# Performance work log

Measured on AMD Instinct MI355X. Metric: run time of the kernel, lower is better.

## Reference

```python
import jax, jax.numpy as jnp
import numpy as np

N_NODES = 100000
N_FEAT = 500
N_HID = 16
N_CLS = 7
N_EDGES = 3200000


def setup_inputs() -> dict:
    key = jax.random.key(0)
    k1, k2, k3, k4 = jax.random.split(key, 4)
    x = jax.random.normal(k1, (N_NODES, N_FEAT), dtype=jnp.float32)
    edge_index = jax.random.randint(k2, (2, N_EDGES), 0, N_NODES, dtype=jnp.int32)
    # Glorot-style init for the two GCNConv weight matrices
    W1 = jax.random.normal(k3, (N_FEAT, N_HID), dtype=jnp.float32) * (1.0 / np.sqrt(N_FEAT))
    b1 = jnp.zeros((N_HID,), dtype=jnp.float32)
    W2 = jax.random.normal(k4, (N_HID, N_CLS), dtype=jnp.float32) * (1.0 / np.sqrt(N_HID))
    b2 = jnp.zeros((N_CLS,), dtype=jnp.float32)
    return {"x": x, "edge_index": edge_index, "W1": W1, "b1": b1, "W2": W2, "b2": b2}


def _gcn_norm(edge_index, n_nodes):
    # Add self-loops, compute symmetric normalization D^-1/2 (A+I) D^-1/2
    loop = jnp.arange(n_nodes, dtype=edge_index.dtype)
    src = jnp.concatenate([edge_index[0], loop])  # [E+N]
    dst = jnp.concatenate([edge_index[1], loop])  # [E+N]
    deg = jax.ops.segment_sum(jnp.ones_like(dst, dtype=jnp.float32), dst, num_segments=n_nodes)
    dinv = jnp.where(deg > 0, jax.lax.rsqrt(deg), 0.0)
    norm = dinv[src] * dinv[dst]  # [E+N]
    return src, dst, norm


def _gcn_conv(h, W, b, src, dst, norm, n_nodes):
    m = h @ W                                   # [N, out] dense projection first (small out dim)
    agg = jax.ops.segment_sum(m[src] * norm[:, None], dst, num_segments=n_nodes)
    return agg + b


def reference(x, edge_index, W1, b1, W2, b2):
    n = x.shape[0]
    src, dst, norm = _gcn_norm(edge_index, n)
    h = jax.nn.relu(_gcn_conv(x, W1, b1, src, dst, norm, n))
    # dropout is identity in eval mode (training=False)
    logits = _gcn_conv(h, W2, b2, src, dst, norm, n)
    return jax.nn.log_softmax(logits, axis=1)
```

## Files before the change

### kernel.cpp

```cpp
#include <hip/hip_runtime.h>
#include <math.h>

#define N_NODES 100000
#define N_EDGES 3200000
#define N_FEAT  500
#define N_HID   16
#define N_CLS   7

#define BKT_SHIFT 7
#define BKT_SIZE  128
#define NBKT      782
#define NBLK_BIN  256
#define EDGES_PER_BLK 12500
#define COUNTS_LEN (NBKT * NBLK_BIN)
#define NBLK_SCANA (COUNTS_LEN / 256)
#define SBUF_CAP  5632

#define OFF_DINV   0
#define OFF_COUNTS 100000
#define OFF_BSUM   300192
#define OFF_ROWP   301216
#define OFF_BINNED 401220
#define OFF_SORTED 3601220
#define OFF_WP     6801220
#define OFF_M1S    6809412
#define OFF_M2S    7609412

typedef __attribute__((ext_vector_type(8))) short short8v;
typedef __attribute__((ext_vector_type(4))) float f32x4v;

__device__ inline unsigned short f2bf(float f) {
    unsigned int u = __float_as_uint(f);
    return (unsigned short)((u + 0x7FFF + ((u >> 16) & 1)) >> 16);
}
__device__ inline float bf2f(unsigned short h) {
    return __uint_as_float((unsigned int)h << 16);
}

__global__ __launch_bounds__(1024) void hist(const int* __restrict__ dst,
                                             int* __restrict__ counts) {
    __shared__ int cnt[4][NBKT];
    int t = threadIdx.x, b = blockIdx.x;
    int wq = (t >> 6) & 3;
    for (int i = t; i < 4 * NBKT; i += 1024) ((int*)cnt)[i] = 0;
    __syncthreads();
    const int4* d4 = (const int4*)(dst + b * EDGES_PER_BLK);
    for (int k = t; k < EDGES_PER_BLK / 4; k += 1024) {
        int4 d = d4[k];
        atomicAdd(&cnt[wq][d.x >> BKT_SHIFT], 1);
        atomicAdd(&cnt[wq][d.y >> BKT_SHIFT], 1);
        atomicAdd(&cnt[wq][d.z >> BKT_SHIFT], 1);
        atomicAdd(&cnt[wq][d.w >> BKT_SHIFT], 1);
    }
    __syncthreads();
    for (int i = t; i < NBKT; i += 1024)
        counts[i * NBLK_BIN + b] = cnt[0][i] + cnt[1][i] + cnt[2][i] + cnt[3][i];
}

__global__ void scanA(int* __restrict__ counts, int* __restrict__ bsum) {
    __shared__ int s[256];
    int t = threadIdx.x;
    int i = blockIdx.x * 256 + t;
    int v = counts[i];
    s[t] = v;
    __syncthreads();
    for (int off = 1; off < 256; off <<= 1) {
        int a = (t >= off) ? s[t - off] : 0;
        __syncthreads();
        s[t] += a;
        __syncthreads();
    }
    counts[i] = s[t] - v;
    if (t == 255) bsum[blockIdx.x] = s[255];
}

__global__ void scanB_wpack(int* __restrict__ bsum, const float* __restrict__ W1,
                            uint4* __restrict__ wp) {
    int t = threadIdx.x;
    {
        int p = t;
        int s = p >> 6, l = p & 63;
        int col = l & 15, kb = s * 32 + (l >> 4) * 8;
        unsigned int hw[4], lw[4];
#pragma unroll
        for (int d = 0; d < 4; ++d) {
            unsigned int hpair = 0, lpair = 0;
#pragma unroll
            for (int e = 0; e < 2; ++e) {
                int k = kb + d * 2 + e;
                float w0 = (k < N_FEAT) ? W1[k * 16 + col] : 0.f;
                unsigned int u = __float_as_uint(w0);
                unsigned int uh = u & 0xFFFF0000u;
                float res = w0 - __uint_as_float(uh);
                hpair |= (uh >> 16) << (16 * e);
                lpair |= (unsigned int)f2bf(res) << (16 * e);
            }
            hw[d] = hpair; lw[d] = lpair;
        }
        wp[p] = make_uint4(hw[0], hw[1], hw[2], hw[3]);
        wp[1024 + p] = make_uint4(lw[0], lw[1], lw[2], lw[3]);
    }
    __shared__ int s[1024];
    int v = (t < NBLK_SCANA) ? bsum[t] : 0;
    s[t] = v;
    __syncthreads();
    for (int off = 1; off < 1024; off <<= 1) {
        int a = (t >= off) ? s[t - off] : 0;
        __syncthreads();
        s[t] += a;
        __syncthreads();
    }
    if (t < NBLK_SCANA) bsum[t] = s[t] - v;
}

__global__ __launch_bounds__(1024) void binpass(const int* __restrict__ src,
                        const int* __restrict__ dst,
                        const int* __restrict__ counts, const int* __restrict__ bsum,
                        unsigned int* __restrict__ binned) {
    __shared__ int cur[NBKT];
    int t = threadIdx.x, b = blockIdx.x;
    for (int i = t; i < NBKT; i += 1024) cur[i] = counts[i * NBLK_BIN + b] + bsum[i];
    __syncthreads();
    const int4* s4 = (const int4*)(src + b * EDGES_PER_BLK);
    const int4* d4 = (const int4*)(dst + b * EDGES_PER_BLK);
    for (int k = t; k < EDGES_PER_BLK / 4; k += 1024) {
        int4 d = d4[k];
        int4 s = s4[k];
        int pos;
        pos = atomicAdd(&cur[d.x >> BKT_SHIFT], 1);
        binned[pos] = (unsigned int)s.x | ((unsigned int)(d.x & (BKT_SIZE - 1)) << 17);
        pos = atomicAdd(&cur[d.y >> BKT_SHIFT], 1);
        binned[pos] = (unsigned int)s.y | ((unsigned int)(d.y & (BKT_SIZE - 1)) << 17);
        pos = atomicAdd(&cur[d.z >> BKT_SHIFT], 1);
        binned[pos] = (unsigned int)s.z | ((unsigned int)(d.z & (BKT_SIZE - 1)) << 17);
        pos = atomicAdd(&cur[d.w >> BKT_SHIFT], 1);
        binned[pos] = (unsigned int)s.w | ((unsigned int)(d.w & (BKT_SIZE - 1)) << 17);
    }
}

__global__ __launch_bounds__(512) void sortA(const unsigned int* __restrict__ binned,
        const int* __restrict__ counts, const int* __restrict__ bsum,
        int* __restrict__ rowptr, float* __restrict__ dinv) {
    __shared__ int cnt[BKT_SIZE];
    __shared__ int sc[BKT_SIZE];
    int t = threadIdx.x, b = blockIdx.x;
    int beg = counts[b * NBLK_BIN] + bsum[b];
    int end = (b < NBKT - 1) ? counts[(b + 1) * NBLK_BIN] + bsum[b + 1] : N_EDGES;
    if (t < BKT_SIZE) cnt[t] = 0;
    __syncthreads();
    for (int e = beg + t; e < end; e += 512)
        atomicAdd(&cnt[(binned[e] >> 17) & (BKT_SIZE - 1)], 1);
    __syncthreads();
    int v = (t < BKT_SIZE) ? cnt[t] : 0;
    if (t < BKT_SIZE) sc[t] = v;
    __syncthreads();
    for (int off = 1; off < BKT_SIZE; off <<= 1) {
        int a = (t < BKT_SIZE && t >= off) ? sc[t - off] : 0;
        __syncthreads();
        if (t < BKT_SIZE) sc[t] += a;
        __syncthreads();
    }
    if (t < BKT_SIZE) {
        int g = b * BKT_SIZE + t;
        if (g < N_NODES) {
            rowptr[g] = beg + sc[t] - v;
            dinv[g] = rsqrtf((float)v + 1.0f);
        }
    }
    if (b == 0 && t == 0) rowptr[N_NODES] = N_EDGES;
}

#define G1_NBLK 1563

__device__ inline void split8(const float4 a, const float4 b, short8v& hi, short8v& lo) {
    float f[8] = {a.x, a.y, a.z, a.w, b.x, b.y, b.z, b.w};
#pragma unroll
    for (int i = 0; i < 8; ++i) {
        unsigned int u = __float_as_uint(f[i]);
        unsigned int uh = u & 0xFFFF0000u;
        hi[i] = (short)(u >> 16);
        lo[i] = (short)f2bf(f[i] - __uint_as_float(uh));
    }
}

__global__ __launch_bounds__(256) void gemm1(const float* __restrict__ x,
        const uint4* __restrict__ wp, const float* __restrict__ dinv,
        unsigned short* __restrict__ m1s) {
    __shared__ uint4 swp[2048];
    const int t = threadIdx.x, b = blockIdx.x;
    const int lane = t & 63, w = t >> 6;
#pragma unroll
    for (int i = 0; i < 8; ++i) swp[i * 256 + t] = wp[i * 256 + t];
    __syncthreads();

    const int r16 = lane & 15, g = lane >> 4;
    const int rowbase = b * 64 + w * 16;
    const int row = rowbase + r16;
    const int srow = (row < N_NODES) ? row : 0;
    const float* pA = x + (size_t)srow * N_FEAT + g * 8;
    const float* t0 = (g <= 2) ? pA + 480 : x;
    const float* t1 = (g <= 1) ? pA + 484 : x;

    float4 a0_0 = *(const float4*)(pA);        float4 a1_0 = *(const float4*)(pA + 4);
    float4 a0_1 = *(const float4*)(pA + 32);   float4 a1_1 = *(const float4*)(pA + 36);
    float4 a0_2 = *(const float4*)(pA + 64);   float4 a1_2 = *(const float4*)(pA + 68);
    float4 a0_3 = *(const float4*)(pA + 96);   float4 a1_3 = *(const float4*)(pA + 100);
    float4 a0_4 = *(const float4*)(pA + 128);  float4 a1_4 = *(const float4*)(pA + 132);
    float4 a0_5 = *(const float4*)(pA + 160);  float4 a1_5 = *(const float4*)(pA + 164);

    f32x4v acc = {0.f, 0.f, 0.f, 0.f};
#pragma unroll
    for (int s = 0; s < 16; ++s) {
        float4 xa, xb;
        switch (s % 6) {
            case 0: xa = a0_0; xb = a1_0; break;
            case 1: xa = a0_1; xb = a1_1; break;
            case 2: xa = a0_2; xb = a1_2; break;
            case 3: xa = a0_3; xb = a1_3; break;
            case 4: xa = a0_4; xb = a1_4; break;
            default: xa = a0_5; xb = a1_5; break;
        }
        if (s <= 9) {
            int tg = s + 6;
            const float* p = (tg == 15) ? t0 : pA + tg * 32;
            const float* q = (tg == 15) ? t1 : pA + tg * 32 + 4;
            float4 n0 = *(const float4*)p;
            float4 n1 = *(const float4*)q;
            switch (s % 6) {
                case 0: a0_0 = n0; a1_0 = n1; break;
                case 1: a0_1 = n0; a1_1 = n1; break;
                case 2: a0_2 = n0; a1_2 = n1; break;
                case 3: a0_3 = n0; a1_3 = n1; break;
                case 4: a0_4 = n0; a1_4 = n1; break;
                default: a0_5 = n0; a1_5 = n1; break;
            }
        }
        short8v ah, al;
        split8(xa, xb, ah, al);
        short8v bh = *reinterpret_cast<const short8v*>(&swp[s * 64 + lane]);
        short8v bl = *reinterpret_cast<const short8v*>(&swp[1024 + s * 64 + lane]);
        acc = __builtin_amdgcn_mfma_f32_16x16x32_bf16(ah, bh, acc, 0, 0, 0);
        acc = __builtin_amdgcn_mfma_f32_16x16x32_bf16(al, bh, acc, 0, 0, 0);
        acc = __builtin_amdgcn_mfma_f32_16x16x32_bf16(ah, bl, acc, 0, 0, 0);
    }

#pragma unroll
    for (int j = 0; j < 4; ++j) {
        int r = rowbase + g * 4 + j;
        if (r < N_NODES) m1s[(size_t)r * 16 + r16] = f2bf(acc[j] * dinv[r]);
    }
}

__global__ __launch_bounds__(512) void sortAgg1(const unsigned int* __restrict__ binned,
        const int* __restrict__ counts, const int* __restrict__ bsum,
        const int* __restrict__ rowptr, const float* __restrict__ dinv,
        const unsigned short* __restrict__ m1s, const float* __restrict__ b1,
        const float* __restrict__ W2, unsigned int* __restrict__ sorted,
        unsigned short* __restrict__ m2s) {
    __shared__ unsigned int sbuf[SBUF_CAP];
    __shared__ int cur[BKT_SIZE];
    __shared__ float acc[BKT_SIZE * 17];
    __shared__ float sW2[N_HID * N_CLS];
    __shared__ float sb1[N_HID];
    int t = threadIdx.x, b = blockIdx.x;
    if (t < N_HID * N_CLS) sW2[t] = W2[t];
    if (t < N_HID) sb1[t] = b1[t];
    int beg = counts[b * NBLK_BIN] + bsum[b];
    int end = (b < NBKT - 1) ? counts[(b + 1) * NBLK_BIN] + bsum[b + 1] : N_EDGES;
    if (t < BKT_SIZE) {
        int g = b * BKT_SIZE + t;
        cur[t] = ((g < N_NODES) ? rowptr[g] : end) - beg;
    }
    __syncthreads();
    for (int e = beg + t; e < end; e += 512) {
        unsigned int u = binned[e];
        int pos = atomicAdd(&cur[(u >> 17) & (BKT_SIZE - 1)], 1);
        if (pos < SBUF_CAP) sbuf[pos] = u & 0x1FFFF;
    }
    __syncthreads();
    int n = end - beg;
    for (int i = t; i < n; i += 512) sorted[beg + i] = sbuf[i];
    {
        int nn = t >> 2, q = t & 3;
        int g = b * BKT_SIZE + nn;
        float a0 = 0.f, a1 = 0.f, a2 = 0.f, a3 = 0.f;
        if (g < N_NODES) {
            int lbeg = rowptr[g] - beg;
            int lend = ((g + 1 <= N_NODES) ? rowptr[g + 1] : N_EDGES) - beg;
            int p = lbeg;
            for (; p + 3 < lend; p += 4) {
                unsigned int s0 = sbuf[p], s1 = sbuf[p + 1];
                unsigned int s2 = sbuf[p + 2], s3 = sbuf[p + 3];
                uint2 w0 = *(const uint2*)&m1s[(size_t)s0 * 16 + q * 4];
                uint2 w1 = *(const uint2*)&m1s[(size_t)s1 * 16 + q * 4];
                uint2 w2 = *(const uint2*)&m1s[(size_t)s2 * 16 + q * 4];
                uint2 w3 = *(const uint2*)&m1s[(size_t)s3 * 16 + q * 4];
                a0 += __uint_as_float(w0.x << 16);
                a1 += __uint_as_float(w0.x & 0xFFFF0000u);
                a2 += __uint_as_float(w0.y << 16);
                a3 += __uint_as_float(w0.y & 0xFFFF0000u);
                a0 += __uint_as_float(w1.x << 16);
                a1 += __uint_as_float(w1.x & 0xFFFF0000u);
                a2 += __uint_as_float(w1.y << 16);
                a3 += __uint_as_float(w1.y & 0xFFFF0000u);
                a0 += __uint_as_float(w2.x << 16);
                a1 += __uint_as_float(w2.x & 0xFFFF0000u);
                a2 += __uint_as_float(w2.y << 16);
                a3 += __uint_as_float(w2.y & 0xFFFF0000u);
                a0 += __uint_as_float(w3.x << 16);
                a1 += __uint_as_float(w3.x & 0xFFFF0000u);
                a2 += __uint_as_float(w3.y << 16);
                a3 += __uint_as_float(w3.y & 0xFFFF0000u);
            }
            for (; p < lend; ++p) {
                unsigned int s0 = sbuf[p];
                uint2 w0 = *(const uint2*)&m1s[(size_t)s0 * 16 + q * 4];
                a0 += __uint_as_float(w0.x << 16);
                a1 += __uint_as_float(w0.x & 0xFFFF0000u);
                a2 += __uint_as_float(w0.y << 16);
                a3 += __uint_as_float(w0.y & 0xFFFF0000u);
            }
        }
        __syncthreads();
        float* ap = &acc[nn * 17 + q * 4];
        ap[0] = a0; ap[1] = a1; ap[2] = a2; ap[3] = a3;
    }
    __syncthreads();
    for (int idx = t; idx < BKT_SIZE * 16; idx += 512) {
        int nn = idx >> 4, jj = idx & 15;
        int gg = b * BKT_SIZE + nn;
        if (gg < N_NODES) {
            float di = dinv[gg];
            float hv = di * (acc[nn * 17 + jj] + bf2f(m1s[(size_t)gg * 16 + jj])) + sb1[jj];
            acc[nn * 17 + jj] = hv > 0.f ? hv : 0.f;
        }
    }
    __syncthreads();
    for (int idx = t; idx < BKT_SIZE * 8; idx += 512) {
        int nn = idx >> 3, cc = idx & 7;
        int gg = b * BKT_SIZE + nn;
        if (gg < N_NODES) {
            float sum = 0.f;
            if (cc < N_CLS) {
#pragma unroll
                for (int jj = 0; jj < N_HID; ++jj) sum += acc[nn * 17 + jj] * sW2[jj * 7 + cc];
                sum *= dinv[gg];
            }
            m2s[(size_t)gg * 8 + cc] = f2bf(sum);
        }
    }
}

__global__ __launch_bounds__(512) void agg2(const unsigned int* __restrict__ sorted,
        const int* __restrict__ rowptr, const float* __restrict__ dinv,
        const unsigned short* __restrict__ m2s, const float* __restrict__ b2,
        float* __restrict__ out) {
    __shared__ float acc[BKT_SIZE * 9];
    int t = threadIdx.x, b = blockIdx.x;
    int n = t >> 2, q = t & 3;
    int g = b * BKT_SIZE + n;
    float a0 = 0.f, a1 = 0.f;
    if (g < N_NODES) {
        int beg = rowptr[g], end = rowptr[g + 1];
        int p = beg;
        for (; p + 3 < end; p += 4) {
            unsigned int s0 = sorted[p], s1 = sorted[p + 1];
            unsigned int s2 = sorted[p + 2], s3 = sorted[p + 3];
            unsigned int w0 = *(const unsigned int*)&m2s[(size_t)s0 * 8 + q * 2];
            unsigned int w1 = *(const unsigned int*)&m2s[(size_t)s1 * 8 + q * 2];
            unsigned int w2 = *(const unsigned int*)&m2s[(size_t)s2 * 8 + q * 2];
            unsigned int w3 = *(const unsigned int*)&m2s[(size_t)s3 * 8 + q * 2];
            a0 += __uint_as_float(w0 << 16); a1 += __uint_as_float(w0 & 0xFFFF0000u);
            a0 += __uint_as_float(w1 << 16); a1 += __uint_as_float(w1 & 0xFFFF0000u);
            a0 += __uint_as_float(w2 << 16); a1 += __uint_as_float(w2 & 0xFFFF0000u);
            a0 += __uint_as_float(w3 << 16); a1 += __uint_as_float(w3 & 0xFFFF0000u);
        }
        for (; p < end; ++p) {
            unsigned int s0 = sorted[p];
            unsigned int w0 = *(const unsigned int*)&m2s[(size_t)s0 * 8 + q * 2];
            a0 += __uint_as_float(w0 << 16); a1 += __uint_as_float(w0 & 0xFFFF0000u);
        }
    }
    float* ap = &acc[n * 9 + q * 2];
    ap[0] = a0; ap[1] = a1;
    __syncthreads();
    int j = t & 7;
    for (int pass = 0; pass < 2; ++pass) {
        int nn = (t >> 3) + pass * 64;
        int gg = b * BKT_SIZE + nn;
        bool valid = (gg < N_NODES) && (j < N_CLS);
        float v = -1e30f;
        if (valid) {
            float di = dinv[gg];
            v = di * (acc[nn * 9 + j] + bf2f(m2s[(size_t)gg * 8 + j])) + b2[j];
        }
        float mx = v;
#pragma unroll
        for (int off = 1; off < 8; off <<= 1) mx = fmaxf(mx, __shfl_xor(mx, off, 8));
        float ex = valid ? expf(v - mx) : 0.f;
        float sum = ex;
#pragma unroll
        for (int off = 1; off < 8; off <<= 1) sum += __shfl_xor(sum, off, 8);
        float ls = mx + logf(sum);
        if (valid) out[(size_t)gg * 7 + j] = v - ls;
    }
}

extern "C" void kernel_launch(void* const* d_in, const int* in_sizes, int n_in,
                              void* d_out, int out_size, void* d_ws, size_t ws_size,
                              hipStream_t stream) {
    const float* x  = (const float*)d_in[0];
    const int*   ei = (const int*)d_in[1];
    const float* W1 = (const float*)d_in[2];
    const float* b1 = (const float*)d_in[3];
    const float* W2 = (const float*)d_in[4];
    const float* b2 = (const float*)d_in[5];
    float* out = (float*)d_out;
    char*  wsb = (char*)d_ws;

    const int* src = ei;
    const int* dst = ei + N_EDGES;

    float*          dinv   = (float*)wsb + OFF_DINV;
    int*            counts = (int*)wsb + OFF_COUNTS;
    int*            bsum   = (int*)wsb + OFF_BSUM;
    int*            rowptr = (int*)wsb + OFF_ROWP;
    unsigned int*   binned = (unsigned int*)wsb + OFF_BINNED;
    unsigned int*   sorted = (unsigned int*)wsb + OFF_SORTED;
    uint4*          wp     = (uint4*)((int*)wsb + OFF_WP);
    unsigned short* m1s    = (unsigned short*)(wsb + (size_t)OFF_M1S * 4);
    unsigned short* m2s    = (unsigned short*)(wsb + (size_t)OFF_M2S * 4);

    hist       <<<NBLK_BIN, 1024, 0, stream>>>(dst, counts);
    scanA      <<<NBLK_SCANA, 256, 0, stream>>>(counts, bsum);
    scanB_wpack<<<1, 1024, 0, stream>>>(bsum, W1, wp);
    binpass    <<<NBLK_BIN, 1024, 0, stream>>>(src, dst, counts, bsum, binned);
    sortA      <<<NBKT, 512, 0, stream>>>(binned, counts, bsum, rowptr, dinv);
    gemm1      <<<G1_NBLK, 256, 0, stream>>>(x, wp, dinv, m1s);
    sortAgg1   <<<NBKT, 512, 0, stream>>>(binned, counts, bsum, rowptr, dinv,
                                          m1s, b1, W2, sorted, m2s);
    agg2       <<<NBKT, 512, 0, stream>>>(sorted, rowptr, dinv, m2s, b2, out);
}
```

Before: 419.4 us.

## Transpose bucket-count layout for per-bucket scans; vectorize agg2 index loads

The count matrix is now stored block-major, so hist and binpass access it contiguously. scanA runs one block per bucket, scanning that bucket's counts across the 256 bin blocks, and bsum becomes the bucket start offsets. sortA and sortAgg1 then read bucket boundaries straight from bsum and no longer need counts. agg2 also peels its edge loop up to a 4-aligned start so it can load four source indices with a single uint4; the scanA reads become strided in exchange.

```diff
diff --git a/kernel.cpp b/kernel.cpp
--- a/kernel.cpp
+++ b/kernel.cpp
@@ -13,7 +13,7 @@
 #define NBLK_BIN  256
 #define EDGES_PER_BLK 12500
 #define COUNTS_LEN (NBKT * NBLK_BIN)
-#define NBLK_SCANA (COUNTS_LEN / 256)
+#define NBLK_SCANA NBKT
 #define SBUF_CAP  5632
 
 #define OFF_DINV   0
@@ -54,14 +54,13 @@
     }
     __syncthreads();
     for (int i = t; i < NBKT; i += 1024)
-        counts[i * NBLK_BIN + b] = cnt[0][i] + cnt[1][i] + cnt[2][i] + cnt[3][i];
+        counts[b * NBKT + i] = cnt[0][i] + cnt[1][i] + cnt[2][i] + cnt[3][i];
 }
 
 __global__ void scanA(int* __restrict__ counts, int* __restrict__ bsum) {
     __shared__ int s[256];
-    int t = threadIdx.x;
-    int i = blockIdx.x * 256 + t;
-    int v = counts[i];
+    int t = threadIdx.x, k = blockIdx.x;
+    int v = counts[t * NBKT + k];
     s[t] = v;
     __syncthreads();
     for (int off = 1; off < 256; off <<= 1) {
@@ -70,8 +69,8 @@
         s[t] += a;
         __syncthreads();
     }
-    counts[i] = s[t] - v;
-    if (t == 255) bsum[blockIdx.x] = s[255];
+    counts[t * NBKT + k] = s[t] - v;
+    if (t == 255) bsum[k] = s[255];
 }
 
 __global__ void scanB_wpack(int* __restrict__ bsum, const float* __restrict__ W1,
@@ -101,7 +100,7 @@
         wp[1024 + p] = make_uint4(lw[0], lw[1], lw[2], lw[3]);
     }
     __shared__ int s[1024];
-    int v = (t < NBLK_SCANA) ? bsum[t] : 0;
+    int v = (t < NBKT) ? bsum[t] : 0;
     s[t] = v;
     __syncthreads();
     for (int off = 1; off < 1024; off <<= 1) {
@@ -110,7 +109,7 @@
         s[t] += a;
         __syncthreads();
     }
-    if (t < NBLK_SCANA) bsum[t] = s[t] - v;
+    if (t < NBKT) bsum[t] = s[t] - v;
 }
 
 __global__ __launch_bounds__(1024) void binpass(const int* __restrict__ src,
@@ -119,7 +118,7 @@
                         unsigned int* __restrict__ binned) {
     __shared__ int cur[NBKT];
     int t = threadIdx.x, b = blockIdx.x;
-    for (int i = t; i < NBKT; i += 1024) cur[i] = counts[i * NBLK_BIN + b] + bsum[i];
+    for (int i = t; i < NBKT; i += 1024) cur[i] = counts[b * NBKT + i] + bsum[i];
     __syncthreads();
     const int4* s4 = (const int4*)(src + b * EDGES_PER_BLK);
     const int4* d4 = (const int4*)(dst + b * EDGES_PER_BLK);
@@ -139,13 +138,13 @@
 }
 
 __global__ __launch_bounds__(512) void sortA(const unsigned int* __restrict__ binned,
-        const int* __restrict__ counts, const int* __restrict__ bsum,
+        const int* __restrict__ bsum,
         int* __restrict__ rowptr, float* __restrict__ dinv) {
     __shared__ int cnt[BKT_SIZE];
     __shared__ int sc[BKT_SIZE];
     int t = threadIdx.x, b = blockIdx.x;
-    int beg = counts[b * NBLK_BIN] + bsum[b];
-    int end = (b < NBKT - 1) ? counts[(b + 1) * NBLK_BIN] + bsum[b + 1] : N_EDGES;
+    int beg = bsum[b];
+    int end = (b < NBKT - 1) ? bsum[b + 1] : N_EDGES;
     if (t < BKT_SIZE) cnt[t] = 0;
     __syncthreads();
     for (int e = beg + t; e < end; e += 512)
@@ -252,7 +251,7 @@
 }
 
 __global__ __launch_bounds__(512) void sortAgg1(const unsigned int* __restrict__ binned,
-        const int* __restrict__ counts, const int* __restrict__ bsum,
+        const int* __restrict__ bsum,
         const int* __restrict__ rowptr, const float* __restrict__ dinv,
         const unsigned short* __restrict__ m1s, const float* __restrict__ b1,
         const float* __restrict__ W2, unsigned int* __restrict__ sorted,
@@ -265,8 +264,8 @@
     int t = threadIdx.x, b = blockIdx.x;
     if (t < N_HID * N_CLS) sW2[t] = W2[t];
     if (t < N_HID) sb1[t] = b1[t];
-    int beg = counts[b * NBLK_BIN] + bsum[b];
-    int end = (b < NBKT - 1) ? counts[(b + 1) * NBLK_BIN] + bsum[b + 1] : N_EDGES;
+    int beg = bsum[b];
+    int end = (b < NBKT - 1) ? bsum[b + 1] : N_EDGES;
     if (t < BKT_SIZE) {
         int g = b * BKT_SIZE + t;
         cur[t] = ((g < N_NODES) ? rowptr[g] : end) - beg;
@@ -363,13 +362,17 @@
     if (g < N_NODES) {
         int beg = rowptr[g], end = rowptr[g + 1];
         int p = beg;
+        for (; (p & 3) && p < end; ++p) {
+            unsigned int s0 = sorted[p];
+            unsigned int w0 = *(const unsigned int*)&m2s[(size_t)s0 * 8 + q * 2];
+            a0 += __uint_as_float(w0 << 16); a1 += __uint_as_float(w0 & 0xFFFF0000u);
+        }
         for (; p + 3 < end; p += 4) {
-            unsigned int s0 = sorted[p], s1 = sorted[p + 1];
-            unsigned int s2 = sorted[p + 2], s3 = sorted[p + 3];
-            unsigned int w0 = *(const unsigned int*)&m2s[(size_t)s0 * 8 + q * 2];
-            unsigned int w1 = *(const unsigned int*)&m2s[(size_t)s1 * 8 + q * 2];
-            unsigned int w2 = *(const unsigned int*)&m2s[(size_t)s2 * 8 + q * 2];
-            unsigned int w3 = *(const unsigned int*)&m2s[(size_t)s3 * 8 + q * 2];
+            uint4 sv = *(const uint4*)&sorted[p];
+            unsigned int w0 = *(const unsigned int*)&m2s[(size_t)sv.x * 8 + q * 2];
+            unsigned int w1 = *(const unsigned int*)&m2s[(size_t)sv.y * 8 + q * 2];
+            unsigned int w2 = *(const unsigned int*)&m2s[(size_t)sv.z * 8 + q * 2];
+            unsigned int w3 = *(const unsigned int*)&m2s[(size_t)sv.w * 8 + q * 2];
             a0 += __uint_as_float(w0 << 16); a1 += __uint_as_float(w0 & 0xFFFF0000u);
             a0 += __uint_as_float(w1 << 16); a1 += __uint_as_float(w1 & 0xFFFF0000u);
             a0 += __uint_as_float(w2 << 16); a1 += __uint_as_float(w2 & 0xFFFF0000u);
@@ -435,9 +438,9 @@
     scanA      <<<NBLK_SCANA, 256, 0, stream>>>(counts, bsum);
     scanB_wpack<<<1, 1024, 0, stream>>>(bsum, W1, wp);
     binpass    <<<NBLK_BIN, 1024, 0, stream>>>(src, dst, counts, bsum, binned);
-    sortA      <<<NBKT, 512, 0, stream>>>(binned, counts, bsum, rowptr, dinv);
+    sortA      <<<NBKT, 512, 0, stream>>>(binned, bsum, rowptr, dinv);
     gemm1      <<<G1_NBLK, 256, 0, stream>>>(x, wp, dinv, m1s);
-    sortAgg1   <<<NBKT, 512, 0, stream>>>(binned, counts, bsum, rowptr, dinv,
+    sortAgg1   <<<NBKT, 512, 0, stream>>>(binned, bsum, rowptr, dinv,
                                           m1s, b1, W2, sorted, m2s);
     agg2       <<<NBKT, 512, 0, stream>>>(sorted, rowptr, dinv, m2s, b2, out);
 }
```

Measured after the change: 418.2 us. About the same (-0.3%).
